# Performance work log

Measured on AMD Instinct MI355X. Metric: run time of the kernel, lower is better.

Reference implementation:

```python
import jax, jax.numpy as jnp
import numpy as np

EMBED_DIM = 768
NUM_HEADS = 8
HEAD_DIM = EMBED_DIM // NUM_HEADS
SCALE = HEAD_DIM ** -0.5
B = 256
N_TOTAL = 16384


def setup_inputs() -> dict:
    key = jax.random.key(0)
    ks = jax.random.split(key, 10)
    s = 1.0 / np.sqrt(EMBED_DIM)
    inp = {
        "query": jax.random.normal(ks[0], (B, EMBED_DIM), jnp.float32),
        "search": jax.random.normal(ks[1], (N_TOTAL, EMBED_DIM), jnp.float32),
        # q_proj / k_proj: Linear(embed_dim, embed_dim)
        "Wq": jax.random.uniform(ks[2], (EMBED_DIM, EMBED_DIM), jnp.float32, -s, s),
        "bq": jax.random.uniform(ks[3], (EMBED_DIM,), jnp.float32, -s, s),
        "Wk": jax.random.uniform(ks[4], (EMBED_DIM, EMBED_DIM), jnp.float32, -s, s),
        "bk": jax.random.uniform(ks[5], (EMBED_DIM,), jnp.float32, -s, s),
        # score_fusion: Linear(H, H//2) -> GELU -> Linear(H//2, 1)
        "W1": jax.random.uniform(ks[6], (NUM_HEADS // 2, NUM_HEADS), jnp.float32, -1.0 / np.sqrt(NUM_HEADS), 1.0 / np.sqrt(NUM_HEADS)),
        "b1": jax.random.uniform(ks[7], (NUM_HEADS // 2,), jnp.float32, -1.0 / np.sqrt(NUM_HEADS), 1.0 / np.sqrt(NUM_HEADS)),
        "W2": jax.random.uniform(ks[8], (1, NUM_HEADS // 2), jnp.float32, -1.0 / np.sqrt(NUM_HEADS // 2), 1.0 / np.sqrt(NUM_HEADS // 2)),
        "b2": jax.random.uniform(ks[9], (1,), jnp.float32, -1.0 / np.sqrt(NUM_HEADS // 2), 1.0 / np.sqrt(NUM_HEADS // 2)),
    }
    return inp


def reference(query, search, Wq, bq, Wk, bk, W1, b1, W2, b2):
    Bq = query.shape[0]
    Nt = search.shape[0]
    # projections -> (B, H, hd) and (N, H, hd)
    q = (query @ Wq.T + bq).reshape(Bq, NUM_HEADS, HEAD_DIM)
    k = (search @ Wk.T + bk).reshape(Nt, NUM_HEADS, HEAD_DIM)
    # per-head dot products: (B, N, H)
    attn_logits = jnp.einsum('bhd,nhd->bnh', q, k) * SCALE
    # tiny MLP over head axis: H -> H//2 -> 1, exact (erf) GELU as in torch default
    h = jax.nn.gelu(attn_logits @ W1.T + b1, approximate=False)
    scores = h @ W2.T + b2  # (B, N, 1)
    return scores.squeeze(-1)
```

## Files before the change

### kernel.cpp

```cpp
#include <hip/hip_runtime.h>
#include <math.h>

#define SCALE 0.1020620726159658f

typedef __attribute__((ext_vector_type(8))) short shortx8;
typedef __attribute__((ext_vector_type(4))) float floatx4;

__device__ __forceinline__ float bf2f(unsigned short u) {
  union { unsigned int i; float f; } c; c.i = ((unsigned int)u) << 16; return c.f;
}
__device__ __forceinline__ unsigned short f2bf(float f) {
  union { float f; unsigned int i; } c; c.f = f;
  unsigned int x = c.i;
  x += 0x7fffu + ((x >> 16) & 1u);
  return (unsigned short)(x >> 16);
}
__device__ __forceinline__ float gelu_fast(float x) {
  float x2 = x * x;
  float y = x * (0.7978845608f + 0.0356774081f * x2);
  float e = fminf(y * 2.885390082f, 60.0f);
  float t = exp2f(e);
  return x * t * __builtin_amdgcn_rcpf(t + 1.0f);
}
__device__ __forceinline__ void async_ld16(const unsigned short* g, unsigned short* l) {
  __builtin_amdgcn_global_load_lds(
      (const __attribute__((address_space(1))) unsigned int*)g,
      (__attribute__((address_space(3))) unsigned int*)l, 16, 0, 0);
}

template <int EPI>
__global__ __launch_bounds__(256) void gemm_bt(
    const unsigned short* __restrict__ A,
    const void* __restrict__ B,
    void* __restrict__ Cout,
    const void* __restrict__ p0, const void* __restrict__ p1,
    void* __restrict__ p2, const void* __restrict__ p3,
    int bconv, int M, int N, int K)
{
  __shared__ unsigned short As[128 * 64];
  __shared__ unsigned short Bs[128 * 64];
  const int tid = threadIdx.x;
  const int wave = tid >> 6;
  const int lane = tid & 63;
  const int wr = wave >> 1, wc = wave & 1;
  const int m0 = blockIdx.y * 128;
  const int n0 = blockIdx.x * 128;

  floatx4 acc[4][4];
#pragma unroll
  for (int i = 0; i < 4; i++)
#pragma unroll
    for (int j = 0; j < 4; j++) acc[i][j] = (floatx4){0.f, 0.f, 0.f, 0.f};

  const int rl = lane >> 3;
  const int cl = (lane & 7) ^ rl;
  const unsigned short* gA[4];
  const unsigned short* gB[4];
  unsigned short* lA[4];
  unsigned short* lB[4];
#pragma unroll
  for (int t = 0; t < 4; t++) {
    int r = wave * 32 + t * 8 + rl;
    gA[t] = A + (size_t)(m0 + r) * K + cl * 8;
    gB[t] = (const unsigned short*)B + (size_t)(n0 + r) * K + cl * 8;
    lA[t] = As + (wave * 32 + t * 8) * 64;
    lB[t] = Bs + (wave * 32 + t * 8) * 64;
  }
  const int cL = lane & 7;
  const int quad = lane >> 4;
  const int l15 = lane & 15;

  for (int k0 = 0; k0 < K; k0 += 64) {
#pragma unroll
    for (int t = 0; t < 4; t++) async_ld16(gA[t] + k0, lA[t]);
    if (!bconv) {
#pragma unroll
      for (int t = 0; t < 4; t++) async_ld16(gB[t] + k0, lB[t]);
    } else {
      const float* Bf = (const float*)B;
#pragma unroll
      for (int t = 0; t < 4; t++) {
        int r = wave * 32 + t * 8 + rl;
        int p = cL ^ rl;
        const float4* src = (const float4*)(Bf + (size_t)(n0 + r) * K + k0 + cL * 8);
        float4 f0 = src[0], f1 = src[1];
        shortx8 vb;
        vb[0] = (short)f2bf(f0.x); vb[1] = (short)f2bf(f0.y);
        vb[2] = (short)f2bf(f0.z); vb[3] = (short)f2bf(f0.w);
        vb[4] = (short)f2bf(f1.x); vb[5] = (short)f2bf(f1.y);
        vb[6] = (short)f2bf(f1.z); vb[7] = (short)f2bf(f1.w);
        *(shortx8*)(Bs + r * 64 + p * 8) = vb;
      }
    }
    __syncthreads();
#pragma unroll
    for (int ks = 0; ks < 2; ks++) {
      shortx8 af[4], bfr[4];
#pragma unroll
      for (int mt = 0; mt < 4; mt++) {
        int r = wr * 64 + mt * 16 + l15;
        int ch = (ks * 4 + quad) ^ (r & 7);
        af[mt] = *(const shortx8*)(As + r * 64 + ch * 8);
      }
#pragma unroll
      for (int nt = 0; nt < 4; nt++) {
        int r = wc * 64 + nt * 16 + l15;
        int ch = (ks * 4 + quad) ^ (r & 7);
        bfr[nt] = *(const shortx8*)(Bs + r * 64 + ch * 8);
      }
#pragma unroll
      for (int mt = 0; mt < 4; mt++)
#pragma unroll
        for (int nt = 0; nt < 4; nt++)
          acc[mt][nt] = __builtin_amdgcn_mfma_f32_16x16x32_bf16(
              af[mt], bfr[nt], acc[mt][nt], 0, 0, 0);
    }
    __syncthreads();
  }

  const int lrow = quad * 4;
  if constexpr (EPI == 0) {
    const float* bqv = (const float*)p0;
    const float* W1f = (const float*)p1;
    float* qf = (float*)p2;
    unsigned short* QWo = (unsigned short*)Cout;
#pragma unroll
    for (int mt = 0; mt < 4; mt++)
#pragma unroll
      for (int nt = 0; nt < 4; nt++) {
        int gm = m0 + wr * 64 + mt * 16 + lrow;
        int gn = n0 + wc * 64 + nt * 16 + l15;
        float bz = bqv[gn];
        int h = gn / 96;
        float w1h0 = W1f[h], w1h1 = W1f[8 + h], w1h2 = W1f[16 + h], w1h3 = W1f[24 + h];
#pragma unroll
        for (int r = 0; r < 4; r++) {
          float qv = acc[mt][nt][r] + bz;
          qf[(size_t)(gm + r) * N + gn] = qv;
          size_t base = (size_t)((gm + r) * 4) * N + gn;
          QWo[base]         = f2bf(SCALE * w1h0 * qv);
          QWo[base + N]     = f2bf(SCALE * w1h1 * qv);
          QWo[base + 2 * N] = f2bf(SCALE * w1h2 * qv);
          QWo[base + 3 * N] = f2bf(SCALE * w1h3 * qv);
        }
      }
  } else if constexpr (EPI == 1) {
    unsigned short* Cb = (unsigned short*)Cout;
#pragma unroll
    for (int mt = 0; mt < 4; mt++)
#pragma unroll
      for (int nt = 0; nt < 4; nt++) {
        int gm = m0 + wr * 64 + mt * 16 + lrow;
        int gn = n0 + wc * 64 + nt * 16 + l15;
#pragma unroll
        for (int r = 0; r < 4; r++)
          Cb[(size_t)(gm + r) * N + gn] = f2bf(acc[mt][nt][r]);
      }
  } else {
    const float* cp = (const float*)p0;
    const float* W2f = (const float*)p1;
    const float* b2f = (const float*)p3;
    float* Co = (float*)Cout;
    float w2v0 = W2f[0], w2v1 = W2f[1], w2v2 = W2f[2], w2v3 = W2f[3];
    float b2v = b2f[0];
#pragma unroll
    for (int mt = 0; mt < 4; mt++) {
      int gm = m0 + wr * 64 + mt * 16 + lrow;
      float cpv0 = cp[gm], cpv1 = cp[gm + 1], cpv2 = cp[gm + 2], cpv3 = cp[gm + 3];
#pragma unroll
      for (int nt = 0; nt < 4; nt++) {
        int gn = n0 + wc * 64 + nt * 16 + l15;
        floatx4 v = acc[mt][nt];
        float s = b2v;
        s += w2v0 * gelu_fast(v[0] + cpv0);
        s += w2v1 * gelu_fast(v[1] + cpv1);
        s += w2v2 * gelu_fast(v[2] + cpv2);
        s += w2v3 * gelu_fast(v[3] + cpv3);
        Co[(size_t)(gm >> 2) * N + gn] = s;
      }
    }
  }
}

__device__ __forceinline__ void cvt8(const float* __restrict__ src,
                                     unsigned short* __restrict__ dst, size_t i) {
  float4 a = *(const float4*)(src + i);
  float4 b = *(const float4*)(src + i + 4);
  shortx8 v;
  v[0] = (short)f2bf(a.x); v[1] = (short)f2bf(a.y);
  v[2] = (short)f2bf(a.z); v[3] = (short)f2bf(a.w);
  v[4] = (short)f2bf(b.x); v[5] = (short)f2bf(b.y);
  v[6] = (short)f2bf(b.z); v[7] = (short)f2bf(b.w);
  *(shortx8*)(dst + i) = v;
}

__global__ __launch_bounds__(256) void prep(
    const float* __restrict__ query, const float* __restrict__ Wq,
    const float* __restrict__ Wk, const float* __restrict__ search,
    unsigned short* __restrict__ qb, unsigned short* __restrict__ wqb,
    unsigned short* __restrict__ WkT, unsigned short* __restrict__ sb)
{
  int b = blockIdx.x, t = threadIdx.x;
  if (b < 576) {
    __shared__ unsigned short tile[32][33];
    int bx = b % 24, by = b / 24;
    int tx = t & 31, ty = t >> 5;
#pragma unroll
    for (int i = 0; i < 4; i++)
      tile[ty + i * 8][tx] = f2bf(Wk[(size_t)(by * 32 + ty + i * 8) * 768 + bx * 32 + tx]);
    __syncthreads();
#pragma unroll
    for (int i = 0; i < 4; i++)
      WkT[(size_t)(bx * 32 + ty + i * 8) * 768 + by * 32 + tx] = tile[tx][ty + i * 8];
  } else if (b < 672) {
    cvt8(query, qb, (size_t)(b - 576) * 2048 + t * 8);
  } else if (b < 960) {
    cvt8(Wq, wqb, (size_t)(b - 672) * 2048 + t * 8);
  } else {
    cvt8(search, sb, (size_t)(b - 960) * 2048 + t * 8);
  }
}

__global__ __launch_bounds__(256) void finish_cp(
    const float* __restrict__ qf, const float* __restrict__ W1f,
    const float* __restrict__ b1f, const float* __restrict__ bkf,
    float* __restrict__ cp)
{
  int b = blockIdx.x, t = threadIdx.x;
  __shared__ float red[768];
  __shared__ float hcs[8];
  const float* qrow = qf + (size_t)b * 768;
  for (int e = t; e < 768; e += 256) red[e] = qrow[e] * bkf[e];
  __syncthreads();
  if (t < 8) {
    float s = 0.f;
    for (int d = 0; d < 96; d++) s += red[t * 96 + d];
    hcs[t] = s;
  }
  __syncthreads();
  if (t < 4) {
    float s = b1f[t];
#pragma unroll
    for (int h = 0; h < 8; h++) s += SCALE * W1f[t * 8 + h] * hcs[h];
    cp[b * 4 + t] = s;
  }
}

extern "C" void kernel_launch(void* const* d_in, const int* in_sizes, int n_in,
                              void* d_out, int out_size, void* d_ws, size_t ws_size,
                              hipStream_t stream) {
  const float* query  = (const float*)d_in[0];
  const float* search = (const float*)d_in[1];
  const float* Wq     = (const float*)d_in[2];
  const float* bq     = (const float*)d_in[3];
  const float* Wk     = (const float*)d_in[4];
  const float* bk     = (const float*)d_in[5];
  const float* W1     = (const float*)d_in[6];
  const float* b1     = (const float*)d_in[7];
  const float* W2     = (const float*)d_in[8];
  const float* b2     = (const float*)d_in[9];

  char* ws = (char*)d_ws;
  float*          cp  = (float*)ws;
  float*          qf  = (float*)(ws + 4096);
  unsigned short* qb  = (unsigned short*)(ws + 790528);
  unsigned short* wqb = (unsigned short*)(ws + 1183744);
  unsigned short* WkT = (unsigned short*)(ws + 2363392);
  unsigned short* QW  = (unsigned short*)(ws + 3543040);
  unsigned short* QQ  = (unsigned short*)(ws + 5115904);
  unsigned short* sb  = (unsigned short*)(ws + 6688768);
  const int use_sb = (ws_size >= 31854592) ? 1 : 0;

  prep<<<use_sb ? 7104 : 960, 256, 0, stream>>>(query, Wq, Wk, search, qb, wqb, WkT, sb);
  gemm_bt<0><<<dim3(6, 2), 256, 0, stream>>>(qb, wqb, QW, bq, W1, qf, nullptr,
                                             0, 256, 768, 768);
  finish_cp<<<256, 256, 0, stream>>>(qf, W1, b1, bk, cp);
  gemm_bt<1><<<dim3(6, 8), 256, 0, stream>>>(QW, WkT, QQ, nullptr, nullptr, nullptr,
                                             nullptr, 0, 1024, 768, 768);
  if (use_sb)
    gemm_bt<2><<<dim3(128, 8), 256, 0, stream>>>(QQ, sb, d_out, cp, W2, nullptr,
                                                 (void*)b2, 0, 1024, 16384, 768);
  else
    gemm_bt<2><<<dim3(128, 8), 256, 0, stream>>>(QQ, search, d_out, cp, W2, nullptr,
                                                 (void*)b2, 1, 1024, 16384, 768);
}
```

Before: 181.0 us.

## Fuse prep kernels into fewer launches and swizzle main GEMM tile order

Cuts the pipeline from five launches to three. The q-projection GEMM now converts fp32 inputs to bf16 inline and runs inside the prep kernel alongside the Wk transpose and search conversion. The bias-correction reduction is folded into the QW·WkT GEMM launch as extra blocks using wave shuffles. The main GEMM remaps block ids so neighbouring blocks share N-tiles, aiming at better L2 reuse. The costs are that the 12 q-projection blocks sit in the same launch as thousands of conversion blocks, and the q-projection blocks stage from fp32 synchronously.

```diff
diff --git a/kernel.cpp b/kernel.cpp
--- a/kernel.cpp
+++ b/kernel.cpp
@@ -27,161 +27,6 @@
       (const __attribute__((address_space(1))) unsigned int*)g,
       (__attribute__((address_space(3))) unsigned int*)l, 16, 0, 0);
 }
-
-template <int EPI>
-__global__ __launch_bounds__(256) void gemm_bt(
-    const unsigned short* __restrict__ A,
-    const void* __restrict__ B,
-    void* __restrict__ Cout,
-    const void* __restrict__ p0, const void* __restrict__ p1,
-    void* __restrict__ p2, const void* __restrict__ p3,
-    int bconv, int M, int N, int K)
-{
-  __shared__ unsigned short As[128 * 64];
-  __shared__ unsigned short Bs[128 * 64];
-  const int tid = threadIdx.x;
-  const int wave = tid >> 6;
-  const int lane = tid & 63;
-  const int wr = wave >> 1, wc = wave & 1;
-  const int m0 = blockIdx.y * 128;
-  const int n0 = blockIdx.x * 128;
-
-  floatx4 acc[4][4];
-#pragma unroll
-  for (int i = 0; i < 4; i++)
-#pragma unroll
-    for (int j = 0; j < 4; j++) acc[i][j] = (floatx4){0.f, 0.f, 0.f, 0.f};
-
-  const int rl = lane >> 3;
-  const int cl = (lane & 7) ^ rl;
-  const unsigned short* gA[4];
-  const unsigned short* gB[4];
-  unsigned short* lA[4];
-  unsigned short* lB[4];
-#pragma unroll
-  for (int t = 0; t < 4; t++) {
-    int r = wave * 32 + t * 8 + rl;
-    gA[t] = A + (size_t)(m0 + r) * K + cl * 8;
-    gB[t] = (const unsigned short*)B + (size_t)(n0 + r) * K + cl * 8;
-    lA[t] = As + (wave * 32 + t * 8) * 64;
-    lB[t] = Bs + (wave * 32 + t * 8) * 64;
-  }
-  const int cL = lane & 7;
-  const int quad = lane >> 4;
-  const int l15 = lane & 15;
-
-  for (int k0 = 0; k0 < K; k0 += 64) {
-#pragma unroll
-    for (int t = 0; t < 4; t++) async_ld16(gA[t] + k0, lA[t]);
-    if (!bconv) {
-#pragma unroll
-      for (int t = 0; t < 4; t++) async_ld16(gB[t] + k0, lB[t]);
-    } else {
-      const float* Bf = (const float*)B;
-#pragma unroll
-      for (int t = 0; t < 4; t++) {
-        int r = wave * 32 + t * 8 + rl;
-        int p = cL ^ rl;
-        const float4* src = (const float4*)(Bf + (size_t)(n0 + r) * K + k0 + cL * 8);
-        float4 f0 = src[0], f1 = src[1];
-        shortx8 vb;
-        vb[0] = (short)f2bf(f0.x); vb[1] = (short)f2bf(f0.y);
-        vb[2] = (short)f2bf(f0.z); vb[3] = (short)f2bf(f0.w);
-        vb[4] = (short)f2bf(f1.x); vb[5] = (short)f2bf(f1.y);
-        vb[6] = (short)f2bf(f1.z); vb[7] = (short)f2bf(f1.w);
-        *(shortx8*)(Bs + r * 64 + p * 8) = vb;
-      }
-    }
-    __syncthreads();
-#pragma unroll
-    for (int ks = 0; ks < 2; ks++) {
-      shortx8 af[4], bfr[4];
-#pragma unroll
-      for (int mt = 0; mt < 4; mt++) {
-        int r = wr * 64 + mt * 16 + l15;
-        int ch = (ks * 4 + quad) ^ (r & 7);
-        af[mt] = *(const shortx8*)(As + r * 64 + ch * 8);
-      }
-#pragma unroll
-      for (int nt = 0; nt < 4; nt++) {
-        int r = wc * 64 + nt * 16 + l15;
-        int ch = (ks * 4 + quad) ^ (r & 7);
-        bfr[nt] = *(const shortx8*)(Bs + r * 64 + ch * 8);
-      }
-#pragma unroll
-      for (int mt = 0; mt < 4; mt++)
-#pragma unroll
-        for (int nt = 0; nt < 4; nt++)
-          acc[mt][nt] = __builtin_amdgcn_mfma_f32_16x16x32_bf16(
-              af[mt], bfr[nt], acc[mt][nt], 0, 0, 0);
-    }
-    __syncthreads();
-  }
-
-  const int lrow = quad * 4;
-  if constexpr (EPI == 0) {
-    const float* bqv = (const float*)p0;
-    const float* W1f = (const float*)p1;
-    float* qf = (float*)p2;
-    unsigned short* QWo = (unsigned short*)Cout;
-#pragma unroll
-    for (int mt = 0; mt < 4; mt++)
-#pragma unroll
-      for (int nt = 0; nt < 4; nt++) {
-        int gm = m0 + wr * 64 + mt * 16 + lrow;
-        int gn = n0 + wc * 64 + nt * 16 + l15;
-        float bz = bqv[gn];
-        int h = gn / 96;
-        float w1h0 = W1f[h], w1h1 = W1f[8 + h], w1h2 = W1f[16 + h], w1h3 = W1f[24 + h];
-#pragma unroll
-        for (int r = 0; r < 4; r++) {
-          float qv = acc[mt][nt][r] + bz;
-          qf[(size_t)(gm + r) * N + gn] = qv;
-          size_t base = (size_t)((gm + r) * 4) * N + gn;
-          QWo[base]         = f2bf(SCALE * w1h0 * qv);
-          QWo[base + N]     = f2bf(SCALE * w1h1 * qv);
-          QWo[base + 2 * N] = f2bf(SCALE * w1h2 * qv);
-          QWo[base + 3 * N] = f2bf(SCALE * w1h3 * qv);
-        }
-      }
-  } else if constexpr (EPI == 1) {
-    unsigned short* Cb = (unsigned short*)Cout;
-#pragma unroll
-    for (int mt = 0; mt < 4; mt++)
-#pragma unroll
-      for (int nt = 0; nt < 4; nt++) {
-        int gm = m0 + wr * 64 + mt * 16 + lrow;
-        int gn = n0 + wc * 64 + nt * 16 + l15;
-#pragma unroll
-        for (int r = 0; r < 4; r++)
-          Cb[(size_t)(gm + r) * N + gn] = f2bf(acc[mt][nt][r]);
-      }
-  } else {
-    const float* cp = (const float*)p0;
-    const float* W2f = (const float*)p1;
-    const float* b2f = (const float*)p3;
-    float* Co = (float*)Cout;
-    float w2v0 = W2f[0], w2v1 = W2f[1], w2v2 = W2f[2], w2v3 = W2f[3];
-    float b2v = b2f[0];
-#pragma unroll
-    for (int mt = 0; mt < 4; mt++) {
-      int gm = m0 + wr * 64 + mt * 16 + lrow;
-      float cpv0 = cp[gm], cpv1 = cp[gm + 1], cpv2 = cp[gm + 2], cpv3 = cp[gm + 3];
-#pragma unroll
-      for (int nt = 0; nt < 4; nt++) {
-        int gn = n0 + wc * 64 + nt * 16 + l15;
-        floatx4 v = acc[mt][nt];
-        float s = b2v;
-        s += w2v0 * gelu_fast(v[0] + cpv0);
-        s += w2v1 * gelu_fast(v[1] + cpv1);
-        s += w2v2 * gelu_fast(v[2] + cpv2);
-        s += w2v3 * gelu_fast(v[3] + cpv3);
-        Co[(size_t)(gm >> 2) * N + gn] = s;
-      }
-    }
-  }
-}
-
 __device__ __forceinline__ void cvt8(const float* __restrict__ src,
                                      unsigned short* __restrict__ dst, size_t i) {
   float4 a = *(const float4*)(src + i);
@@ -193,18 +38,106 @@
   v[6] = (short)f2bf(b.z); v[7] = (short)f2bf(b.w);
   *(shortx8*)(dst + i) = v;
 }
-
-__global__ __launch_bounds__(256) void prep(
+__device__ __forceinline__ void stage_f32(const float* __restrict__ src, int ldk,
+                                          unsigned short* __restrict__ lds,
+                                          int wave, int lane, int row0, int k0) {
+  int rl = lane >> 3, cL = lane & 7;
+#pragma unroll
+  for (int t = 0; t < 4; t++) {
+    int r = wave * 32 + t * 8 + rl;
+    int p = cL ^ rl;
+    const float4* s4 = (const float4*)(src + (size_t)(row0 + r) * ldk + k0 + cL * 8);
+    float4 f0 = s4[0], f1 = s4[1];
+    shortx8 v;
+    v[0] = (short)f2bf(f0.x); v[1] = (short)f2bf(f0.y);
+    v[2] = (short)f2bf(f0.z); v[3] = (short)f2bf(f0.w);
+    v[4] = (short)f2bf(f1.x); v[5] = (short)f2bf(f1.y);
+    v[6] = (short)f2bf(f1.z); v[7] = (short)f2bf(f1.w);
+    *(shortx8*)(lds + r * 64 + p * 8) = v;
+  }
+}
+__device__ __forceinline__ void mfma_consume(const unsigned short* __restrict__ As,
+                                             const unsigned short* __restrict__ Bs,
+                                             int wr, int wc, int quad, int l15,
+                                             floatx4 (&acc)[4][4]) {
+#pragma unroll
+  for (int ks = 0; ks < 2; ks++) {
+    shortx8 af[4], bfr[4];
+#pragma unroll
+    for (int mt = 0; mt < 4; mt++) {
+      int r = wr * 64 + mt * 16 + l15;
+      int ch = (ks * 4 + quad) ^ (r & 7);
+      af[mt] = *(const shortx8*)(As + r * 64 + ch * 8);
+    }
+#pragma unroll
+    for (int nt = 0; nt < 4; nt++) {
+      int r = wc * 64 + nt * 16 + l15;
+      int ch = (ks * 4 + quad) ^ (r & 7);
+      bfr[nt] = *(const shortx8*)(Bs + r * 64 + ch * 8);
+    }
+#pragma unroll
+    for (int mt = 0; mt < 4; mt++)
+#pragma unroll
+      for (int nt = 0; nt < 4; nt++)
+        acc[mt][nt] = __builtin_amdgcn_mfma_f32_16x16x32_bf16(
+            af[mt], bfr[nt], acc[mt][nt], 0, 0, 0);
+  }
+}
+
+__global__ __launch_bounds__(256) void fused_pre(
     const float* __restrict__ query, const float* __restrict__ Wq,
     const float* __restrict__ Wk, const float* __restrict__ search,
-    unsigned short* __restrict__ qb, unsigned short* __restrict__ wqb,
-    unsigned short* __restrict__ WkT, unsigned short* __restrict__ sb)
+    const float* __restrict__ bq, const float* __restrict__ W1,
+    unsigned short* __restrict__ WkT, unsigned short* __restrict__ QW,
+    float* __restrict__ qf, unsigned short* __restrict__ sb)
 {
-  int b = blockIdx.x, t = threadIdx.x;
-  if (b < 576) {
+  const int bid = blockIdx.x, t = threadIdx.x;
+  if (bid < 12) {
+    __shared__ unsigned short As[128 * 64];
+    __shared__ unsigned short Bs[128 * 64];
+    const int bx = bid % 6, by = bid / 6;
+    const int m0 = by * 128, n0 = bx * 128;
+    const int wave = t >> 6, lane = t & 63;
+    const int wr = wave >> 1, wc = wave & 1;
+    const int quad = lane >> 4, l15 = lane & 15;
+    floatx4 acc[4][4];
+#pragma unroll
+    for (int i = 0; i < 4; i++)
+#pragma unroll
+      for (int j = 0; j < 4; j++) acc[i][j] = (floatx4){0.f, 0.f, 0.f, 0.f};
+    for (int k0 = 0; k0 < 768; k0 += 64) {
+      stage_f32(query, 768, As, wave, lane, m0, k0);
+      stage_f32(Wq, 768, Bs, wave, lane, n0, k0);
+      __syncthreads();
+      mfma_consume(As, Bs, wr, wc, quad, l15, acc);
+      __syncthreads();
+    }
+    const int N = 768;
+    const int lrow = quad * 4;
+#pragma unroll
+    for (int mt = 0; mt < 4; mt++)
+#pragma unroll
+      for (int nt = 0; nt < 4; nt++) {
+        int gm = m0 + wr * 64 + mt * 16 + lrow;
+        int gn = n0 + wc * 64 + nt * 16 + l15;
+        float bz = bq[gn];
+        int h = gn / 96;
+        float w1h0 = W1[h], w1h1 = W1[8 + h], w1h2 = W1[16 + h], w1h3 = W1[24 + h];
+#pragma unroll
+        for (int r = 0; r < 4; r++) {
+          float qv = acc[mt][nt][r] + bz;
+          qf[(size_t)(gm + r) * N + gn] = qv;
+          size_t base = (size_t)((gm + r) * 4) * N + gn;
+          QW[base]         = f2bf(SCALE * w1h0 * qv);
+          QW[base + N]     = f2bf(SCALE * w1h1 * qv);
+          QW[base + 2 * N] = f2bf(SCALE * w1h2 * qv);
+          QW[base + 3 * N] = f2bf(SCALE * w1h3 * qv);
+        }
+      }
+  } else if (bid < 588) {
     __shared__ unsigned short tile[32][33];
-    int bx = b % 24, by = b / 24;
-    int tx = t & 31, ty = t >> 5;
+    const int tb = bid - 12, bx = tb % 24, by = tb / 24;
+    const int tx = t & 31, ty = t >> 5;
 #pragma unroll
     for (int i = 0; i < 4; i++)
       tile[ty + i * 8][tx] = f2bf(Wk[(size_t)(by * 32 + ty + i * 8) * 768 + bx * 32 + tx]);
@@ -212,37 +145,151 @@
 #pragma unroll
     for (int i = 0; i < 4; i++)
       WkT[(size_t)(bx * 32 + ty + i * 8) * 768 + by * 32 + tx] = tile[tx][ty + i * 8];
-  } else if (b < 672) {
-    cvt8(query, qb, (size_t)(b - 576) * 2048 + t * 8);
-  } else if (b < 960) {
-    cvt8(Wq, wqb, (size_t)(b - 672) * 2048 + t * 8);
   } else {
-    cvt8(search, sb, (size_t)(b - 960) * 2048 + t * 8);
-  }
-}
-
-__global__ __launch_bounds__(256) void finish_cp(
-    const float* __restrict__ qf, const float* __restrict__ W1f,
-    const float* __restrict__ b1f, const float* __restrict__ bkf,
+    cvt8(search, sb, (size_t)(bid - 588) * 2048 + t * 8);
+  }
+}
+
+__global__ __launch_bounds__(256) void mid(
+    const unsigned short* __restrict__ QW, const unsigned short* __restrict__ WkT,
+    unsigned short* __restrict__ QQ,
+    const float* __restrict__ qf, const float* __restrict__ W1,
+    const float* __restrict__ b1, const float* __restrict__ bk,
     float* __restrict__ cp)
 {
-  int b = blockIdx.x, t = threadIdx.x;
-  __shared__ float red[768];
-  __shared__ float hcs[8];
-  const float* qrow = qf + (size_t)b * 768;
-  for (int e = t; e < 768; e += 256) red[e] = qrow[e] * bkf[e];
-  __syncthreads();
-  if (t < 8) {
-    float s = 0.f;
-    for (int d = 0; d < 96; d++) s += red[t * 96 + d];
-    hcs[t] = s;
-  }
-  __syncthreads();
-  if (t < 4) {
-    float s = b1f[t];
-#pragma unroll
-    for (int h = 0; h < 8; h++) s += SCALE * W1f[t * 8 + h] * hcs[h];
-    cp[b * 4 + t] = s;
+  const int t = threadIdx.x;
+  const int wave = t >> 6, lane = t & 63;
+  if (blockIdx.y < 8) {
+    __shared__ unsigned short As[128 * 64];
+    __shared__ unsigned short Bs[128 * 64];
+    const int m0 = blockIdx.y * 128, n0 = blockIdx.x * 128;
+    const int K = 768, N = 768;
+    const int wr = wave >> 1, wc = wave & 1;
+    const int quad = lane >> 4, l15 = lane & 15;
+    floatx4 acc[4][4];
+#pragma unroll
+    for (int i = 0; i < 4; i++)
+#pragma unroll
+      for (int j = 0; j < 4; j++) acc[i][j] = (floatx4){0.f, 0.f, 0.f, 0.f};
+    const int rl = lane >> 3, cl = (lane & 7) ^ rl;
+    const unsigned short* gA[4];
+    const unsigned short* gB[4];
+    unsigned short* lA[4];
+    unsigned short* lB[4];
+#pragma unroll
+    for (int tt = 0; tt < 4; tt++) {
+      int r = wave * 32 + tt * 8 + rl;
+      gA[tt] = QW + (size_t)(m0 + r) * K + cl * 8;
+      gB[tt] = WkT + (size_t)(n0 + r) * K + cl * 8;
+      lA[tt] = As + (wave * 32 + tt * 8) * 64;
+      lB[tt] = Bs + (wave * 32 + tt * 8) * 64;
+    }
+    for (int k0 = 0; k0 < K; k0 += 64) {
+#pragma unroll
+      for (int tt = 0; tt < 4; tt++) async_ld16(gA[tt] + k0, lA[tt]);
+#pragma unroll
+      for (int tt = 0; tt < 4; tt++) async_ld16(gB[tt] + k0, lB[tt]);
+      __syncthreads();
+      mfma_consume(As, Bs, wr, wc, quad, l15, acc);
+      __syncthreads();
+    }
+    const int lrow = quad * 4;
+#pragma unroll
+    for (int mt = 0; mt < 4; mt++)
+#pragma unroll
+      for (int nt = 0; nt < 4; nt++) {
+        int gm = m0 + wr * 64 + mt * 16 + lrow;
+        int gn = n0 + wc * 64 + nt * 16 + l15;
+#pragma unroll
+        for (int r = 0; r < 4; r++)
+          QQ[(size_t)(gm + r) * N + gn] = f2bf(acc[mt][nt][r]);
+      }
+  } else {
+    const int bstart = blockIdx.x * 43;
+    const int bend = min(bstart + 43, 256);
+    for (int b = bstart + wave; b < bend; b += 4) {
+      const float* qrow = qf + (size_t)b * 768;
+      int e0 = lane * 12;
+      float s = 0.f;
+#pragma unroll
+      for (int i = 0; i < 12; i++) s += qrow[e0 + i] * bk[e0 + i];
+      s += __shfl_xor(s, 1); s += __shfl_xor(s, 2); s += __shfl_xor(s, 4);
+      float v = __shfl(s, (lane & 7) * 8);
+      float w = W1[((lane >> 3) & 3) * 8 + (lane & 7)] * v;
+      w += __shfl_xor(w, 1); w += __shfl_xor(w, 2); w += __shfl_xor(w, 4);
+      if (lane < 32 && (lane & 7) == 0) {
+        int j = lane >> 3;
+        cp[b * 4 + j] = b1[j] + SCALE * w;
+      }
+    }
+  }
+}
+
+__global__ __launch_bounds__(256) void gemm_main(
+    const unsigned short* __restrict__ QQ, const void* __restrict__ Bv,
+    float* __restrict__ out, const float* __restrict__ cp,
+    const float* __restrict__ W2, const float* __restrict__ b2, int bconv)
+{
+  __shared__ unsigned short As[128 * 64];
+  __shared__ unsigned short Bs[128 * 64];
+  const int bid = blockIdx.x;
+  const int n_tile = (bid & 7) * 16 + ((bid >> 3) & 15);
+  const int m_tile = bid >> 7;
+  const int m0 = m_tile * 128, n0 = n_tile * 128;
+  const int K = 768, N = 16384;
+  const int t = threadIdx.x;
+  const int wave = t >> 6, lane = t & 63;
+  const int wr = wave >> 1, wc = wave & 1;
+  const int quad = lane >> 4, l15 = lane & 15;
+  floatx4 acc[4][4];
+#pragma unroll
+  for (int i = 0; i < 4; i++)
+#pragma unroll
+    for (int j = 0; j < 4; j++) acc[i][j] = (floatx4){0.f, 0.f, 0.f, 0.f};
+  const int rl = lane >> 3, cl = (lane & 7) ^ rl;
+  const unsigned short* gA[4];
+  const unsigned short* gB[4];
+  unsigned short* lA[4];
+  unsigned short* lB[4];
+#pragma unroll
+  for (int tt = 0; tt < 4; tt++) {
+    int r = wave * 32 + tt * 8 + rl;
+    gA[tt] = QQ + (size_t)(m0 + r) * K + cl * 8;
+    gB[tt] = (const unsigned short*)Bv + (size_t)(n0 + r) * K + cl * 8;
+    lA[tt] = As + (wave * 32 + tt * 8) * 64;
+    lB[tt] = Bs + (wave * 32 + tt * 8) * 64;
+  }
+  for (int k0 = 0; k0 < K; k0 += 64) {
+#pragma unroll
+    for (int tt = 0; tt < 4; tt++) async_ld16(gA[tt] + k0, lA[tt]);
+    if (!bconv) {
+#pragma unroll
+      for (int tt = 0; tt < 4; tt++) async_ld16(gB[tt] + k0, lB[tt]);
+    } else {
+      stage_f32((const float*)Bv, K, Bs, wave, lane, n0, k0);
+    }
+    __syncthreads();
+    mfma_consume(As, Bs, wr, wc, quad, l15, acc);
+    __syncthreads();
+  }
+  const float w2v0 = W2[0], w2v1 = W2[1], w2v2 = W2[2], w2v3 = W2[3];
+  const float b2v = b2[0];
+  const int lrow = quad * 4;
+#pragma unroll
+  for (int mt = 0; mt < 4; mt++) {
+    int gm = m0 + wr * 64 + mt * 16 + lrow;
+    float cpv0 = cp[gm], cpv1 = cp[gm + 1], cpv2 = cp[gm + 2], cpv3 = cp[gm + 3];
+#pragma unroll
+    for (int nt = 0; nt < 4; nt++) {
+      int gn = n0 + wc * 64 + nt * 16 + l15;
+      floatx4 v = acc[mt][nt];
+      float s = b2v;
+      s += w2v0 * gelu_fast(v[0] + cpv0);
+      s += w2v1 * gelu_fast(v[1] + cpv1);
+      s += w2v2 * gelu_fast(v[2] + cpv2);
+      s += w2v3 * gelu_fast(v[3] + cpv3);
+      out[(size_t)(gm >> 2) * N + gn] = s;
+    }
   }
 }
 
@@ -263,24 +310,15 @@
   char* ws = (char*)d_ws;
   float*          cp  = (float*)ws;
   float*          qf  = (float*)(ws + 4096);
-  unsigned short* qb  = (unsigned short*)(ws + 790528);
-  unsigned short* wqb = (unsigned short*)(ws + 1183744);
-  unsigned short* WkT = (unsigned short*)(ws + 2363392);
-  unsigned short* QW  = (unsigned short*)(ws + 3543040);
-  unsigned short* QQ  = (unsigned short*)(ws + 5115904);
-  unsigned short* sb  = (unsigned short*)(ws + 6688768);
-  const int use_sb = (ws_size >= 31854592) ? 1 : 0;
-
-  prep<<<use_sb ? 7104 : 960, 256, 0, stream>>>(query, Wq, Wk, search, qb, wqb, WkT, sb);
-  gemm_bt<0><<<dim3(6, 2), 256, 0, stream>>>(qb, wqb, QW, bq, W1, qf, nullptr,
-                                             0, 256, 768, 768);
-  finish_cp<<<256, 256, 0, stream>>>(qf, W1, b1, bk, cp);
-  gemm_bt<1><<<dim3(6, 8), 256, 0, stream>>>(QW, WkT, QQ, nullptr, nullptr, nullptr,
-                                             nullptr, 0, 1024, 768, 768);
-  if (use_sb)
-    gemm_bt<2><<<dim3(128, 8), 256, 0, stream>>>(QQ, sb, d_out, cp, W2, nullptr,
-                                                 (void*)b2, 0, 1024, 16384, 768);
-  else
-    gemm_bt<2><<<dim3(128, 8), 256, 0, stream>>>(QQ, search, d_out, cp, W2, nullptr,
-                                                 (void*)b2, 1, 1024, 16384, 768);
-}
+  unsigned short* WkT = (unsigned short*)(ws + 790528);
+  unsigned short* QW  = (unsigned short*)(ws + 1970176);
+  unsigned short* QQ  = (unsigned short*)(ws + 3543040);
+  unsigned short* sb  = (unsigned short*)(ws + 5115904);
+  const int use_sb = (ws_size >= 30281728u) ? 1 : 0;
+
+  fused_pre<<<use_sb ? 6732 : 588, 256, 0, stream>>>(query, Wq, Wk, search,
+                                                     bq, W1, WkT, QW, qf, sb);
+  mid<<<dim3(6, 9), 256, 0, stream>>>(QW, WkT, QQ, qf, W1, b1, bk, cp);
+  gemm_main<<<1024, 256, 0, stream>>>(QQ, use_sb ? (const void*)sb : (const void*)search,
+                                      (float*)d_out, cp, W2, b2, use_sb ? 0 : 1);
+}
```

After: 180.7 us. No clear change (-0.2%).
